# Performance work log

Measured on AMD Instinct MI355X. Metric: run time of the kernel, lower is better.

Reference implementation:

```python
import jax, jax.numpy as jnp
import numpy as np

B, BINS, EMBED, HID, IND = 1, 500, 1024, 512, 128
POOL, MC_CROP, HIC_CROP = 5, 50, 10


def setup_inputs() -> dict:
    key = jax.random.key(0)
    ks = jax.random.split(key, 10)
    def w(k, shape, fan_in):
        return (jax.random.normal(k, shape, jnp.float32) / np.sqrt(fan_in)).astype(jnp.float32)
    return dict(
        x=jax.random.normal(ks[0], (B, BINS, EMBED), jnp.float32),
        # project MLP
        p_w1=w(ks[1], (EMBED, HID), EMBED), p_b1=jnp.zeros((HID,), jnp.float32),
        p_w2=w(ks[2], (HID, HID), HID), p_b2=jnp.zeros((HID,), jnp.float32),
        # pairattn_cop stub: per-pair linears (micro at full res, hic after 5x5 avg-pool)
        micro_w=w(ks[3], (HID, IND), HID), micro_b=jnp.zeros((IND,), jnp.float32),
        hic_w=w(ks[4], (HID, IND), HID), hic_b=jnp.zeros((IND,), jnp.float32),
        # prediction heads
        head_mc_w=w(ks[5], (IND, 2), IND), head_mc_b=jnp.zeros((2,), jnp.float32),
        head_ih_w1=w(ks[6], (IND, IND // 2), IND), head_ih_b1=jnp.zeros((IND // 2,), jnp.float32),
        head_ih_w2=w(ks[7], (IND // 2, 2), IND // 2), head_ih_b2=jnp.zeros((2,), jnp.float32),
        head_hic_w=w(ks[8], (IND, 3), IND), head_hic_b=jnp.zeros((3,), jnp.float32),
    )


def reference(x, p_w1, p_b1, p_w2, p_b2, micro_w, micro_b, hic_w, hic_b,
              head_mc_w, head_mc_b, head_ih_w1, head_ih_b1, head_ih_w2, head_ih_b2,
              head_hic_w, head_hic_b):
    # project: Linear -> ReLU -> Linear
    h = jax.nn.relu(x @ p_w1 + p_b1) @ p_w2 + p_b2            # [B, bins, HID]
    # output_head: fused pairwise outer-sum mean + scaled elementwise dot
    xi = h[:, :, None, :]                                      # [B, bins, 1, HID]
    xj = h[:, None, :, :]                                      # [B, 1, bins, HID]
    pair = (xi + xj) * 0.5 + xi * xj * (1.0 / np.sqrt(HID))    # [B, bins, bins, HID]
    # pairattn_cop stub
    micro = pair @ micro_w + micro_b                           # [B, bins, bins, IND]
    nb = BINS // POOL
    hic_in = pair.reshape(B, nb, POOL, nb, POOL, HID).mean(axis=(2, 4))  # [B, nb, nb, HID]
    hic = hic_in @ hic_w + hic_b                               # [B, nb, nb, IND]
    # prediction heads with crops
    mc = micro[:, MC_CROP:-MC_CROP, MC_CROP:-MC_CROP, :]       # [B, 400, 400, IND]
    out_mc = mc @ head_mc_w + head_mc_b
    out_ih = jax.nn.relu(mc @ head_ih_w1 + head_ih_b1) @ head_ih_w2 + head_ih_b2
    hc = hic[:, HIC_CROP:-HIC_CROP, HIC_CROP:-HIC_CROP, :]     # [B, 80, 80, IND]
    out_hic = hc @ head_hic_w + head_hic_b
    return (out_mc, out_ih, micro, out_hic)
```

## Files before the change

kernel.cpp:

```cpp
#include <hip/hip_runtime.h>

#define BINS 500
#define HID  512
#define INDD 128
#define PAIR_S 0.044194173824159216f

#define OFF_MC    0
#define OFF_IH    320000
#define OFF_MICRO 640000
#define OFF_HIC   32640000

#define WS_U     0
#define WS_MWT   64000
#define WS_HBF   96768
#define WS_H     256000
#define WS_HBAR  512000
#define WS_HWT   563200
#define WS_W1CT  595968

typedef __bf16 bf16;
typedef bf16 bf16x4 __attribute__((ext_vector_type(4)));
typedef bf16 bf16x8 __attribute__((ext_vector_type(8)));
typedef float f32x4 __attribute__((ext_vector_type(4)));

__device__ __forceinline__ bf16x8 join8(bf16x4 lo, bf16x4 hi) {
  return __builtin_shufflevector(lo, hi, 0, 1, 2, 3, 4, 5, 6, 7);
}
__device__ __forceinline__ bf16x4 cvt4(float a, float b, float c, float d) {
  bf16x4 r; r[0] = (bf16)a; r[1] = (bf16)b; r[2] = (bf16)c; r[3] = (bf16)d; return r;
}

__global__ void zero_init(float* __restrict__ ws) {
  int idx = (blockIdx.x * 256 + threadIdx.x) * 4;
  float4 z = {0.f, 0.f, 0.f, 0.f};
  *(float4*)(ws + idx) = z;
  *(float4*)(ws + WS_H + idx) = z;
}

__global__ __launch_bounds__(256, 2)
void gemm_ks(const float* __restrict__ A, const float* __restrict__ B,
             const float* __restrict__ abias, float* __restrict__ C,
             int M, int N, int K_per, int a_relu, float scale) {
  __shared__ float a_lds[64][36];
  __shared__ float bt_lds[64][36];
  const int t = threadIdx.x;
  const int w = t >> 6, l = t & 63;
  const int lr = l & 15, g = l >> 4;
  const int r0 = blockIdx.x * 64, n0 = blockIdx.y * 64;
  const int kbase = blockIdx.z * K_per;
  f32x4 acc[4] = {};
  for (int kq = 0; kq < K_per; kq += 32) {
    const int k0 = kbase + kq;
    {
      int row = t >> 2, kc = (t & 3) * 8;
      int gr = r0 + row; gr = gr < M ? gr : M - 1;
      const float* src = A + (size_t)gr * K_per * gridDim.z + k0 + kc;
      float4 v0 = *(const float4*)src;
      float4 v1 = *(const float4*)(src + 4);
      if (abias) {
        const float* bp = abias + k0 + kc;
        v0.x += bp[0]; v0.y += bp[1]; v0.z += bp[2]; v0.w += bp[3];
        v1.x += bp[4]; v1.y += bp[5]; v1.z += bp[6]; v1.w += bp[7];
        if (a_relu) {
          v0.x = fmaxf(v0.x, 0.f); v0.y = fmaxf(v0.y, 0.f);
          v0.z = fmaxf(v0.z, 0.f); v0.w = fmaxf(v0.w, 0.f);
          v1.x = fmaxf(v1.x, 0.f); v1.y = fmaxf(v1.y, 0.f);
          v1.z = fmaxf(v1.z, 0.f); v1.w = fmaxf(v1.w, 0.f);
        }
      }
      *(float4*)&a_lds[row][kc]     = v0;
      *(float4*)&a_lds[row][kc + 4] = v1;
    }
    {
      int n = t & 63, ks = (t >> 6) * 8;
      const float* src = B + (size_t)(k0 + ks) * N + n0 + n;
      #pragma unroll
      for (int s = 0; s < 8; s++) bt_lds[n][ks + s] = src[(size_t)s * N];
    }
    __syncthreads();
    bf16x8 ahi, alo;
    {
      int row = w * 16 + lr;
      float4 u0 = *(const float4*)&a_lds[row][g * 8];
      float4 u1 = *(const float4*)&a_lds[row][g * 8 + 4];
      float v[8] = {u0.x, u0.y, u0.z, u0.w, u1.x, u1.y, u1.z, u1.w};
      #pragma unroll
      for (int e = 0; e < 8; e++) {
        bf16 h = (bf16)v[e];
        ahi[e] = h; alo[e] = (bf16)(v[e] - (float)h);
      }
    }
    #pragma unroll
    for (int fn = 0; fn < 4; fn++) {
      int col = fn * 16 + lr;
      float4 u0 = *(const float4*)&bt_lds[col][g * 8];
      float4 u1 = *(const float4*)&bt_lds[col][g * 8 + 4];
      float v[8] = {u0.x, u0.y, u0.z, u0.w, u1.x, u1.y, u1.z, u1.w};
      bf16x8 bhi, blo;
      #pragma unroll
      for (int e = 0; e < 8; e++) {
        bf16 h = (bf16)v[e];
        bhi[e] = h; blo[e] = (bf16)(v[e] - (float)h);
      }
      acc[fn] = __builtin_amdgcn_mfma_f32_16x16x32_bf16(ahi, bhi, acc[fn], 0, 0, 0);
      acc[fn] = __builtin_amdgcn_mfma_f32_16x16x32_bf16(ahi, blo, acc[fn], 0, 0, 0);
      acc[fn] = __builtin_amdgcn_mfma_f32_16x16x32_bf16(alo, bhi, acc[fn], 0, 0, 0);
    }
    __syncthreads();
  }
  #pragma unroll
  for (int fn = 0; fn < 4; fn++) {
    int col = n0 + fn * 16 + lr;
    #pragma unroll
    for (int r = 0; r < 4; r++) {
      int row = r0 + w * 16 + g * 4 + r;
      if (row < M) atomicAdd(&C[(size_t)row * N + col], acc[fn][r] * scale);
    }
  }
}

__global__ void post_h(const float* __restrict__ h, const float* __restrict__ b2,
                       const float* __restrict__ micro_w,
                       const float* __restrict__ hic_w, const float* __restrict__ w_ih1,
                       const float* __restrict__ w_mc, float* __restrict__ ws) {
  int g = blockIdx.x * 256 + threadIdx.x;
  if (g < 32000) {
    int e = g * 8, k = e & (HID - 1);
    float4 a0 = *(const float4*)(h + e),  a1 = *(const float4*)(h + e + 4);
    float4 c0 = *(const float4*)(b2 + k), c1 = *(const float4*)(b2 + k + 4);
    bf16x8 o;
    o[0] = (bf16)(a0.x + c0.x); o[1] = (bf16)(a0.y + c0.y);
    o[2] = (bf16)(a0.z + c0.z); o[3] = (bf16)(a0.w + c0.w);
    o[4] = (bf16)(a1.x + c1.x); o[5] = (bf16)(a1.y + c1.y);
    o[6] = (bf16)(a1.z + c1.z); o[7] = (bf16)(a1.w + c1.w);
    *(bf16x8*)((bf16*)(ws + WS_HBF) + e) = o;
  } else if (g < 40192) {
    int gg = (g - 32000) * 8;
    int n = gg >> 9, k = gg & 511;
    bf16x8 o;
    #pragma unroll
    for (int e = 0; e < 8; e++) o[e] = (bf16)(PAIR_S * micro_w[(size_t)(k + e) * INDD + n]);
    *(bf16x8*)((bf16*)(ws + WS_MWT) + gg) = o;
  } else if (g < 46592) {
    int gg = (g - 40192) * 8;
    int a = gg >> 9, k = gg & (HID - 1);
    const float* p = h + (size_t)(a * 5) * HID + k;
    float s[8] = {};
    #pragma unroll
    for (int r = 0; r < 5; r++) {
      float4 v0 = *(const float4*)(p + r * HID);
      float4 v1 = *(const float4*)(p + r * HID + 4);
      s[0] += v0.x; s[1] += v0.y; s[2] += v0.z; s[3] += v0.w;
      s[4] += v1.x; s[5] += v1.y; s[6] += v1.z; s[7] += v1.w;
    }
    float4 c0 = *(const float4*)(b2 + k), c1 = *(const float4*)(b2 + k + 4);
    float4 o0 = {s[0] * 0.2f + c0.x, s[1] * 0.2f + c0.y, s[2] * 0.2f + c0.z, s[3] * 0.2f + c0.w};
    float4 o1 = {s[4] * 0.2f + c1.x, s[5] * 0.2f + c1.y, s[6] * 0.2f + c1.z, s[7] * 0.2f + c1.w};
    *(float4*)(ws + WS_HBAR + gg)     = o0;
    *(float4*)(ws + WS_HBAR + gg + 4) = o1;
  } else if (g < 54784) {
    int gg = (g - 46592) * 8;
    int n = gg >> 9, k = gg & 511;
    bf16x8 o;
    #pragma unroll
    for (int e = 0; e < 8; e++) o[e] = (bf16)hic_w[(size_t)(k + e) * INDD + n];
    *(bf16x8*)((bf16*)(ws + WS_HWT) + gg) = o;
  } else if (g < 56064) {
    int gg = (g - 54784) * 8;
    int n = gg >> 7, k = gg & 127;
    bf16x8 o;
    #pragma unroll
    for (int e = 0; e < 8; e++) {
      float v = 0.f;
      if (n < 64) v = w_ih1[(k + e) * 64 + n];
      else if (n < 66) v = w_mc[(k + e) * 2 + (n - 64)];
      o[e] = (bf16)v;
    }
    *(bf16x8*)((bf16*)(ws + WS_W1CT) + gg) = o;
  } else if (g < 64064) {
    int gg = (g - 56064) * 8;
    float4 z = {0.f, 0.f, 0.f, 0.f};
    *(float4*)(ws + WS_U + gg)     = z;
    *(float4*)(ws + WS_U + gg + 4) = z;
  }
}

__global__ __launch_bounds__(256, 4)
void fused_micro(const float* __restrict__ wsf, const float* __restrict__ micro_b,
                 float* __restrict__ out) {
  __shared__ bf16 Ht[2][128 * 32];
  __shared__ bf16 Bt[2][128 * 32];
  const int t = threadIdx.x;
  const int wv = t >> 6, l = t & 63;
  const int wj = wv >> 1, wn = wv & 1;
  const int lr = l & 15, g = l >> 4;
  const int i  = blockIdx.x;
  const int j0 = blockIdx.y * 128;
  const bf16* Hbf = (const bf16*)(wsf + WS_HBF);
  const bf16* mwt = (const bf16*)(wsf + WS_MWT);
  const float* U  = wsf + WS_U;
  const int bn = t >> 1, bh = t & 1;
  const int arow   = l >> 2;
  const int achunk = (l & 3) ^ ((l >> 3) & 3);
  const bf16* hbi = Hbf + (size_t)i * HID;
  f32x4 acc[4][4] = {};

  #pragma unroll
  for (int q = 0; q < 2; q++) {
    int row = wv * 32 + q * 16 + arow;
    int jj = j0 + row; jj = jj < BINS ? jj : BINS - 1;
    __builtin_amdgcn_global_load_lds(
        (const __attribute__((address_space(1))) void*)(Hbf + (size_t)jj * HID + achunk * 8),
        (__attribute__((address_space(3))) void*)(&Ht[0][(wv * 32 + q * 16) * 32]),
        16, 0, 0);
  }
  {
    bf16x8 w0 = *(const bf16x8*)(mwt + (size_t)bn * HID + bh * 16);
    bf16x8 w1 = *(const bf16x8*)(mwt + (size_t)bn * HID + bh * 16 + 8);
    bf16x8 h0 = *(const bf16x8*)(hbi + bh * 16);
    bf16x8 h1 = *(const bf16x8*)(hbi + bh * 16 + 8);
    bf16x8 o0, o1;
    #pragma unroll
    for (int e = 0; e < 8; e++) o0[e] = (bf16)((float)h0[e] * (float)w0[e]);
    #pragma unroll
    for (int e = 0; e < 8; e++) o1[e] = (bf16)((float)h1[e] * (float)w1[e]);
    const int sw = (bn >> 1) & 3;
    *(bf16x8*)(&Bt[0][0] + bn * 32 + ((bh * 2)     ^ sw) * 8) = o0;
    *(bf16x8*)(&Bt[0][0] + bn * 32 + ((bh * 2 + 1) ^ sw) * 8) = o1;
  }
  asm volatile("s_waitcnt vmcnt(0) lgkmcnt(0)" ::: "memory");
  __builtin_amdgcn_s_barrier();

  int cur = 0;
  for (int kt = 0; kt < 16; kt++) {
    const bf16* htc = &Ht[cur][0];
    const bf16* btc = &Bt[cur][0];
    bf16x8 w0, w1, h0, h1;
    if (kt < 15) {
      const int kn = (kt + 1) * 32;
      w0 = *(const bf16x8*)(mwt + (size_t)bn * HID + kn + bh * 16);
      w1 = *(const bf16x8*)(mwt + (size_t)bn * HID + kn + bh * 16 + 8);
      h0 = *(const bf16x8*)(hbi + kn + bh * 16);
      h1 = *(const bf16x8*)(hbi + kn + bh * 16 + 8);
      #pragma unroll
      for (int q = 0; q < 2; q++) {
        int row = wv * 32 + q * 16 + arow;
        int jj = j0 + row; jj = jj < BINS ? jj : BINS - 1;
        __builtin_amdgcn_global_load_lds(
            (const __attribute__((address_space(1))) void*)(Hbf + (size_t)jj * HID + kn + achunk * 8),
            (__attribute__((address_space(3))) void*)(&Ht[cur ^ 1][(wv * 32 + q * 16) * 32]),
            16, 0, 0);
      }
      asm volatile("s_waitcnt vmcnt(6)" ::: "memory");
    } else {
      asm volatile("s_waitcnt vmcnt(0)" ::: "memory");
    }
    bf16x8 af[4], bfr[4];
    const int s = g ^ ((lr >> 1) & 3);
    #pragma unroll
    for (int fm = 0; fm < 4; fm++)
      af[fm] = *(const bf16x8*)(htc + (wj * 64 + fm * 16 + lr) * 32 + s * 8);
    #pragma unroll
    for (int fn = 0; fn < 4; fn++)
      bfr[fn] = *(const bf16x8*)(btc + (wn * 64 + fn * 16 + lr) * 32 + s * 8);
    #pragma unroll
    for (int fm = 0; fm < 4; fm++)
      #pragma unroll
      for (int fn = 0; fn < 4; fn++)
        acc[fm][fn] = __builtin_amdgcn_mfma_f32_16x16x32_bf16(af[fm], bfr[fn], acc[fm][fn], 0, 0, 0);
    if (kt < 15) {
      bf16x8 o0, o1;
      #pragma unroll
      for (int e = 0; e < 8; e++) o0[e] = (bf16)((float)h0[e] * (float)w0[e]);
      #pragma unroll
      for (int e = 0; e < 8; e++) o1[e] = (bf16)((float)h1[e] * (float)w1[e]);
      bf16* btn = &Bt[cur ^ 1][0];
      const int sw = (bn >> 1) & 3;
      *(bf16x8*)(btn + bn * 32 + ((bh * 2)     ^ sw) * 8) = o0;
      *(bf16x8*)(btn + bn * 32 + ((bh * 2 + 1) ^ sw) * 8) = o1;
    }
    asm volatile("s_waitcnt lgkmcnt(0)" ::: "memory");
    __builtin_amdgcn_s_barrier();
    cur ^= 1;
  }

  float Ui[4];
  #pragma unroll
  for (int fn = 0; fn < 4; fn++) {
    int n = wn * 64 + fn * 16 + lr;
    Ui[fn] = U[(size_t)i * INDD + n] + micro_b[n];
  }
  #pragma unroll
  for (int fm = 0; fm < 4; fm++) {
    #pragma unroll
    for (int r = 0; r < 4; r++) {
      int j = j0 + wj * 64 + fm * 16 + g * 4 + r;
      if (j < BINS) {
        const float* Uj = U + (size_t)j * INDD;
        size_t base = (size_t)OFF_MICRO + ((size_t)i * BINS + j) * INDD;
        #pragma unroll
        for (int fn = 0; fn < 4; fn++) {
          int n = wn * 64 + fn * 16 + lr;
          out[base + n] = acc[fm][fn][r] + Ui[fn] + Uj[n];
        }
      }
    }
  }
}

__global__ __launch_bounds__(256, 3)
void heads_direct(const float* __restrict__ micro, const float* __restrict__ wsf,
                  const float* __restrict__ b1, const float* __restrict__ w2,
                  const float* __restrict__ bmc, const float* __restrict__ b2,
                  float* __restrict__ out) {
  const int t = threadIdx.x;
  const int wv = t >> 6, l = t & 63;
  const int lr = l & 15, g = l >> 4;
  const int mm0 = blockIdx.x * 256;
  const bf16* w1c = (const bf16*)(wsf + WS_W1CT);
  int mrow[4];
  #pragma unroll
  for (int fm = 0; fm < 4; fm++) {
    int mm = mm0 + wv * 64 + fm * 16 + lr;
    mrow[fm] = 25050 + mm + 100 * (mm / 400);
  }
  f32x4 acc[4][5] = {};
  #pragma unroll
  for (int kt = 0; kt < 4; kt++) {
    const int k0 = kt * 32;
    bf16x8 bfr[5];
    #pragma unroll
    for (int fn = 0; fn < 5; fn++) {
      int q = fn * 16 + lr;
      bfr[fn] = *(const bf16x8*)(w1c + q * 128 + k0 + g * 8);
    }
    #pragma unroll
    for (int fm = 0; fm < 4; fm++) {
      const float* src = micro + (size_t)mrow[fm] * INDD + k0 + g * 8;
      float4 v0 = *(const float4*)src;
      float4 v1 = *(const float4*)(src + 4);
      bf16x8 af = join8(cvt4(v0.x, v0.y, v0.z, v0.w), cvt4(v1.x, v1.y, v1.z, v1.w));
      #pragma unroll
      for (int fn = 0; fn < 5; fn++)
        acc[fm][fn] = __builtin_amdgcn_mfma_f32_16x16x32_bf16(af, bfr[fn], acc[fm][fn], 0, 0, 0);
    }
  }
  float w2a[4], w2b[4], b1v[4];
  #pragma unroll
  for (int fn = 0; fn < 4; fn++) {
    int q = fn * 16 + lr;
    w2a[fn] = w2[q * 2]; w2b[fn] = w2[q * 2 + 1]; b1v[fn] = b1[q];
  }
  float bm = (lr < 2) ? bmc[lr] : 0.f;
  float b2a = b2[0], b2bv = b2[1];
  #pragma unroll
  for (int fm = 0; fm < 4; fm++) {
    #pragma unroll
    for (int r = 0; r < 4; r++) {
      int m = wv * 64 + fm * 16 + g * 4 + r;
      float s0 = 0.f, s1 = 0.f;
      #pragma unroll
      for (int fn = 0; fn < 4; fn++) {
        float v = fmaxf(acc[fm][fn][r] + b1v[fn], 0.f);
        s0 += v * w2a[fn]; s1 += v * w2b[fn];
      }
      #pragma unroll
      for (int mk = 1; mk < 16; mk <<= 1) {
        s0 += __shfl_xor(s0, mk);
        s1 += __shfl_xor(s1, mk);
      }
      size_t mo = (size_t)(mm0 + m);
      if (lr == 0) {
        out[OFF_IH + mo * 2]     = s0 + b2a;
        out[OFF_IH + mo * 2 + 1] = s1 + b2bv;
      }
      if (lr < 2) out[OFF_MC + mo * 2 + lr] = acc[fm][4][r] + bm;
    }
  }
}

__device__ __forceinline__ bf16x4 pair4(float4 a, float4 b) {
  bf16x4 r;
  r[0] = (bf16)((a.x + b.x) * 0.5f + a.x * b.x * PAIR_S);
  r[1] = (bf16)((a.y + b.y) * 0.5f + a.y * b.y * PAIR_S);
  r[2] = (bf16)((a.z + b.z) * 0.5f + a.z * b.z * PAIR_S);
  r[3] = (bf16)((a.w + b.w) * 0.5f + a.w * b.w * PAIR_S);
  return r;
}

__global__ __launch_bounds__(256, 2)
void hic_kernel(const float* __restrict__ hbar, const float* __restrict__ wsf,
                const float* __restrict__ hicb, const float* __restrict__ whic,
                const float* __restrict__ bhic, float* __restrict__ out) {
  __shared__ float ha_lds[16][36];
  __shared__ float hb_lds[16][36];
  __shared__ bf16 pair_lds[256][36];
  __shared__ bf16 bt_lds[128][36];
  const int t = threadIdx.x;
  const int wv = t >> 6, l = t & 63;
  const int lr = l & 15, g = l >> 4;
  const int a0 = 10 + blockIdx.x * 16, b0 = 10 + blockIdx.y * 16;
  const bf16* hwt = (const bf16*)(wsf + WS_HWT);
  f32x4 acc[4][8] = {};
  for (int kt = 0; kt < 16; kt++) {
    const int k0 = kt * 32;
    if (t < 64) {
      int row = t >> 2, c = (t & 3) * 8;
      const float* src = hbar + (size_t)(a0 + row) * HID + k0 + c;
      *(float4*)&ha_lds[row][c]     = *(const float4*)src;
      *(float4*)&ha_lds[row][c + 4] = *(const float4*)(src + 4);
    } else if (t < 128) {
      int tt = t - 64;
      int row = tt >> 2, c = (tt & 3) * 8;
      const float* src = hbar + (size_t)(b0 + row) * HID + k0 + c;
      *(float4*)&hb_lds[row][c]     = *(const float4*)src;
      *(float4*)&hb_lds[row][c + 4] = *(const float4*)(src + 4);
    } else {
      int tt = t - 128;
      #pragma unroll
      for (int rep = 0; rep < 4; rep++) {
        int chunk = tt * 4 + rep;
        int n = chunk >> 2, part = chunk & 3;
        bf16x8 v = *(const bf16x8*)(hwt + (size_t)n * HID + k0 + part * 8);
        *(bf16x4*)&bt_lds[n][part * 8]     = __builtin_shufflevector(v, v, 0, 1, 2, 3);
        *(bf16x4*)&bt_lds[n][part * 8 + 4] = __builtin_shufflevector(v, v, 4, 5, 6, 7);
      }
    }
    __syncthreads();
    {
      int m = t;
      const float* pa = &ha_lds[m >> 4][0];
      const float* pb = &hb_lds[m & 15][0];
      #pragma unroll
      for (int c = 0; c < 4; c++) {
        float4 av0 = *(const float4*)(pa + c * 8);
        float4 av1 = *(const float4*)(pa + c * 8 + 4);
        float4 bv0 = *(const float4*)(pb + c * 8);
        float4 bv1 = *(const float4*)(pb + c * 8 + 4);
        *(bf16x4*)&pair_lds[m][c * 8]     = pair4(av0, bv0);
        *(bf16x4*)&pair_lds[m][c * 8 + 4] = pair4(av1, bv1);
      }
    }
    __syncthreads();
    bf16x8 af[4], bfr[8];
    #pragma unroll
    for (int fm = 0; fm < 4; fm++) {
      int row = wv * 64 + fm * 16 + lr;
      af[fm] = join8(*(const bf16x4*)&pair_lds[row][g * 8],
                     *(const bf16x4*)&pair_lds[row][g * 8 + 4]);
    }
    #pragma unroll
    for (int fn = 0; fn < 8; fn++) {
      int col = fn * 16 + lr;
      bfr[fn] = join8(*(const bf16x4*)&bt_lds[col][g * 8],
                      *(const bf16x4*)&bt_lds[col][g * 8 + 4]);
    }
    #pragma unroll
    for (int fm = 0; fm < 4; fm++)
      #pragma unroll
      for (int fn = 0; fn < 8; fn++)
        acc[fm][fn] = __builtin_amdgcn_mfma_f32_16x16x32_bf16(af[fm], bfr[fn], acc[fm][fn], 0, 0, 0);
    __syncthreads();
  }
  float wh0[8], wh1[8], wh2[8], hbv[8];
  #pragma unroll
  for (int fn = 0; fn < 8; fn++) {
    int n = fn * 16 + lr;
    wh0[fn] = whic[n * 3]; wh1[fn] = whic[n * 3 + 1]; wh2[fn] = whic[n * 3 + 2];
    hbv[fn] = hicb[n];
  }
  float bh0 = bhic[0], bh1 = bhic[1], bh2 = bhic[2];
  #pragma unroll
  for (int fm = 0; fm < 4; fm++) {
    #pragma unroll
    for (int r = 0; r < 4; r++) {
      int m = wv * 64 + fm * 16 + g * 4 + r;
      float s0 = 0.f, s1 = 0.f, s2 = 0.f;
      #pragma unroll
      for (int fn = 0; fn < 8; fn++) {
        float v = acc[fm][fn][r] + hbv[fn];
        s0 += v * wh0[fn]; s1 += v * wh1[fn]; s2 += v * wh2[fn];
      }
      #pragma unroll
      for (int mk = 1; mk < 16; mk <<= 1) {
        s0 += __shfl_xor(s0, mk);
        s1 += __shfl_xor(s1, mk);
        s2 += __shfl_xor(s2, mk);
      }
      if (lr == 0) {
        int aa = a0 + (m >> 4) - 10, bb = b0 + (m & 15) - 10;
        size_t o = (size_t)OFF_HIC + (size_t)(aa * 80 + bb) * 3;
        out[o] = s0 + bh0; out[o + 1] = s1 + bh1; out[o + 2] = s2 + bh2;
      }
    }
  }
}

extern "C" void kernel_launch(void* const* d_in, const int* in_sizes, int n_in,
                              void* d_out, int out_size, void* d_ws, size_t ws_size,
                              hipStream_t stream) {
  (void)in_sizes; (void)n_in; (void)out_size; (void)ws_size;
  const float* x    = (const float*)d_in[0];
  const float* pw1  = (const float*)d_in[1];
  const float* pb1  = (const float*)d_in[2];
  const float* pw2  = (const float*)d_in[3];
  const float* pb2  = (const float*)d_in[4];
  const float* mw   = (const float*)d_in[5];
  const float* mb   = (const float*)d_in[6];
  const float* hw   = (const float*)d_in[7];
  const float* hb   = (const float*)d_in[8];
  const float* wmc  = (const float*)d_in[9];
  const float* bmc  = (const float*)d_in[10];
  const float* wih1 = (const float*)d_in[11];
  const float* bih1 = (const float*)d_in[12];
  const float* wih2 = (const float*)d_in[13];
  const float* bih2 = (const float*)d_in[14];
  const float* whic = (const float*)d_in[15];
  const float* bhic = (const float*)d_in[16];
  float* out = (float*)d_out;
  float* ws  = (float*)d_ws;

  zero_init<<<250, 256, 0, stream>>>(ws);
  gemm_ks<<<dim3(8, 8, 8), 256, 0, stream>>>(x, pw1, nullptr, ws, 500, 512, 128, 0, 1.f);
  gemm_ks<<<dim3(8, 8, 4), 256, 0, stream>>>(ws, pw2, pb1, ws + WS_H, 500, 512, 128, 1, 1.f);
  post_h<<<251, 256, 0, stream>>>(ws + WS_H, pb2, mw, hw, wih1, wmc, ws);
  gemm_ks<<<dim3(8, 2, 8), 256, 0, stream>>>(ws + WS_H, mw, pb2, ws + WS_U, 500, 128, 64, 0, 0.5f);
  fused_micro<<<dim3(500, 4), 256, 0, stream>>>(ws, mb, out);
  heads_direct<<<625, 256, 0, stream>>>(out + OFF_MICRO, ws, bih1, wih2, bmc, bih2, out);
  hic_kernel<<<dim3(5, 5), 256, 0, stream>>>(ws + WS_HBAR, ws, hb, whic, bhic, out);
}
```

Before: 157.5 us.

## Replace double-buffered LDS pipeline with single buffer and two barriers per k-step

Removes the double-buffered Ht/Bt shared-memory staging in fused_micro and uses single buffers. Each k-step now issues the async H tile loads and writes the scaled B tile, then syncs, computes the MFMAs and syncs again. This halves LDS use (which may allow more blocks per CU) and simplifies the waitcnt logic. In exchange, the next tile's global loads no longer overlap the current tile's MFMAs, and each iteration pays an extra barrier.

Result: no change. 156.3 us (-0.8%).

```diff
diff --git a/kernel.cpp b/kernel.cpp
--- a/kernel.cpp
+++ b/kernel.cpp
@@ -188,8 +188,8 @@
 __global__ __launch_bounds__(256, 4)
 void fused_micro(const float* __restrict__ wsf, const float* __restrict__ micro_b,
                  float* __restrict__ out) {
-  __shared__ bf16 Ht[2][128 * 32];
-  __shared__ bf16 Bt[2][128 * 32];
+  __shared__ bf16 Ht[128 * 32];
+  __shared__ bf16 Bt[128 * 32];
   const int t = threadIdx.x;
   const int wv = t >> 6, l = t & 63;
   const int wj = wv >> 1, wn = wv & 1;
@@ -205,83 +205,54 @@
   const bf16* hbi = Hbf + (size_t)i * HID;
   f32x4 acc[4][4] = {};
 
-  #pragma unroll
-  for (int q = 0; q < 2; q++) {
-    int row = wv * 32 + q * 16 + arow;
-    int jj = j0 + row; jj = jj < BINS ? jj : BINS - 1;
-    __builtin_amdgcn_global_load_lds(
-        (const __attribute__((address_space(1))) void*)(Hbf + (size_t)jj * HID + achunk * 8),
-        (__attribute__((address_space(3))) void*)(&Ht[0][(wv * 32 + q * 16) * 32]),
-        16, 0, 0);
-  }
-  {
-    bf16x8 w0 = *(const bf16x8*)(mwt + (size_t)bn * HID + bh * 16);
-    bf16x8 w1 = *(const bf16x8*)(mwt + (size_t)bn * HID + bh * 16 + 8);
-    bf16x8 h0 = *(const bf16x8*)(hbi + bh * 16);
-    bf16x8 h1 = *(const bf16x8*)(hbi + bh * 16 + 8);
-    bf16x8 o0, o1;
-    #pragma unroll
-    for (int e = 0; e < 8; e++) o0[e] = (bf16)((float)h0[e] * (float)w0[e]);
-    #pragma unroll
-    for (int e = 0; e < 8; e++) o1[e] = (bf16)((float)h1[e] * (float)w1[e]);
-    const int sw = (bn >> 1) & 3;
-    *(bf16x8*)(&Bt[0][0] + bn * 32 + ((bh * 2)     ^ sw) * 8) = o0;
-    *(bf16x8*)(&Bt[0][0] + bn * 32 + ((bh * 2 + 1) ^ sw) * 8) = o1;
-  }
-  asm volatile("s_waitcnt vmcnt(0) lgkmcnt(0)" ::: "memory");
-  __builtin_amdgcn_s_barrier();
-
-  int cur = 0;
+  bf16x8 w0 = *(const bf16x8*)(mwt + (size_t)bn * HID + bh * 16);
+  bf16x8 w1 = *(const bf16x8*)(mwt + (size_t)bn * HID + bh * 16 + 8);
+  bf16x8 h0 = *(const bf16x8*)(hbi + bh * 16);
+  bf16x8 h1 = *(const bf16x8*)(hbi + bh * 16 + 8);
+
   for (int kt = 0; kt < 16; kt++) {
-    const bf16* htc = &Ht[cur][0];
-    const bf16* btc = &Bt[cur][0];
-    bf16x8 w0, w1, h0, h1;
+    const int k0 = kt * 32;
+    #pragma unroll
+    for (int q = 0; q < 2; q++) {
+      int row = wv * 32 + q * 16 + arow;
+      int jj = j0 + row; jj = jj < BINS ? jj : BINS - 1;
+      __builtin_amdgcn_global_load_lds(
+          (const __attribute__((address_space(1))) void*)(Hbf + (size_t)jj * HID + k0 + achunk * 8),
+          (__attribute__((address_space(3))) void*)(Ht + (wv * 32 + q * 16) * 32),
+          16, 0, 0);
+    }
+    {
+      bf16x8 o0, o1;
+      #pragma unroll
+      for (int e = 0; e < 8; e++) o0[e] = (bf16)((float)h0[e] * (float)w0[e]);
+      #pragma unroll
+      for (int e = 0; e < 8; e++) o1[e] = (bf16)((float)h1[e] * (float)w1[e]);
+      const int sw = (bn >> 1) & 3;
+      *(bf16x8*)(Bt + bn * 32 + ((bh * 2)     ^ sw) * 8) = o0;
+      *(bf16x8*)(Bt + bn * 32 + ((bh * 2 + 1) ^ sw) * 8) = o1;
+    }
     if (kt < 15) {
-      const int kn = (kt + 1) * 32;
+      const int kn = k0 + 32;
       w0 = *(const bf16x8*)(mwt + (size_t)bn * HID + kn + bh * 16);
       w1 = *(const bf16x8*)(mwt + (size_t)bn * HID + kn + bh * 16 + 8);
       h0 = *(const bf16x8*)(hbi + kn + bh * 16);
       h1 = *(const bf16x8*)(hbi + kn + bh * 16 + 8);
-      #pragma unroll
-      for (int q = 0; q < 2; q++) {
-        int row = wv * 32 + q * 16 + arow;
-        int jj = j0 + row; jj = jj < BINS ? jj : BINS - 1;
-        __builtin_amdgcn_global_load_lds(
-            (const __attribute__((address_space(1))) void*)(Hbf + (size_t)jj * HID + kn + achunk * 8),
-            (__attribute__((address_space(3))) void*)(&Ht[cur ^ 1][(wv * 32 + q * 16) * 32]),
-            16, 0, 0);
-      }
-      asm volatile("s_waitcnt vmcnt(6)" ::: "memory");
-    } else {
-      asm volatile("s_waitcnt vmcnt(0)" ::: "memory");
-    }
+    }
+    __syncthreads();
     bf16x8 af[4], bfr[4];
     const int s = g ^ ((lr >> 1) & 3);
     #pragma unroll
     for (int fm = 0; fm < 4; fm++)
-      af[fm] = *(const bf16x8*)(htc + (wj * 64 + fm * 16 + lr) * 32 + s * 8);
+      af[fm] = *(const bf16x8*)(Ht + (wj * 64 + fm * 16 + lr) * 32 + s * 8);
     #pragma unroll
     for (int fn = 0; fn < 4; fn++)
-      bfr[fn] = *(const bf16x8*)(btc + (wn * 64 + fn * 16 + lr) * 32 + s * 8);
+      bfr[fn] = *(const bf16x8*)(Bt + (wn * 64 + fn * 16 + lr) * 32 + s * 8);
     #pragma unroll
     for (int fm = 0; fm < 4; fm++)
       #pragma unroll
       for (int fn = 0; fn < 4; fn++)
         acc[fm][fn] = __builtin_amdgcn_mfma_f32_16x16x32_bf16(af[fm], bfr[fn], acc[fm][fn], 0, 0, 0);
-    if (kt < 15) {
-      bf16x8 o0, o1;
-      #pragma unroll
-      for (int e = 0; e < 8; e++) o0[e] = (bf16)((float)h0[e] * (float)w0[e]);
-      #pragma unroll
-      for (int e = 0; e < 8; e++) o1[e] = (bf16)((float)h1[e] * (float)w1[e]);
-      bf16* btn = &Bt[cur ^ 1][0];
-      const int sw = (bn >> 1) & 3;
-      *(bf16x8*)(btn + bn * 32 + ((bh * 2)     ^ sw) * 8) = o0;
-      *(bf16x8*)(btn + bn * 32 + ((bh * 2 + 1) ^ sw) * 8) = o1;
-    }
-    asm volatile("s_waitcnt lgkmcnt(0)" ::: "memory");
-    __builtin_amdgcn_s_barrier();
-    cur ^= 1;
+    __syncthreads();
   }
 
   float Ui[4];
```

## Prefetch B-operand inputs two stages ahead and prioritize MFMA issue in fused_micro

Applied to the files above, without the earlier changes.

Restructures the K-loop software pipeline in fused_micro. The weight and h values used to build the scaled B tile are now loaded into registers two K-steps ahead. The next B tile is written to LDS before the MFMA block, and the MFMA block is wrapped in s_setprio to raise wave priority. The hand-tuned s_waitcnt/s_barrier pairs become __syncthreads, and launch bounds drop from 4 to 3 waves per SIMD to leave room for the extra prefetch registers. The aim is to hide global load latency behind matrix work. The risks are lower occupancy, and a fence in __syncthreads that may wait on all outstanding loads, including the prefetches.

New measurement: 158.1 us. About the same (+0.4%).

```diff
diff --git a/kernel.cpp b/kernel.cpp
--- a/kernel.cpp
+++ b/kernel.cpp
@@ -185,7 +185,7 @@
   }
 }
 
-__global__ __launch_bounds__(256, 4)
+__global__ __launch_bounds__(256, 3)
 void fused_micro(const float* __restrict__ wsf, const float* __restrict__ micro_b,
                  float* __restrict__ out) {
   __shared__ bf16 Ht[2][128 * 32];
@@ -203,8 +203,24 @@
   const int arow   = l >> 2;
   const int achunk = (l & 3) ^ ((l >> 3) & 3);
   const bf16* hbi = Hbf + (size_t)i * HID;
+  const bf16* wsrc = mwt + (size_t)bn * HID + bh * 16;
+  const bf16* hsrc = hbi + bh * 16;
   f32x4 acc[4][4] = {};
 
+  {
+    bf16x8 w0 = *(const bf16x8*)(wsrc);
+    bf16x8 w1 = *(const bf16x8*)(wsrc + 8);
+    bf16x8 h0 = *(const bf16x8*)(hsrc);
+    bf16x8 h1 = *(const bf16x8*)(hsrc + 8);
+    bf16x8 o0, o1;
+    #pragma unroll
+    for (int e = 0; e < 8; e++) o0[e] = (bf16)((float)h0[e] * (float)w0[e]);
+    #pragma unroll
+    for (int e = 0; e < 8; e++) o1[e] = (bf16)((float)h1[e] * (float)w1[e]);
+    const int sw = (bn >> 1) & 3;
+    *(bf16x8*)(&Bt[0][0] + bn * 32 + ((bh * 2)     ^ sw) * 8) = o0;
+    *(bf16x8*)(&Bt[0][0] + bn * 32 + ((bh * 2 + 1) ^ sw) * 8) = o1;
+  }
   #pragma unroll
   for (int q = 0; q < 2; q++) {
     int row = wv * 32 + q * 16 + arow;
@@ -214,34 +230,24 @@
         (__attribute__((address_space(3))) void*)(&Ht[0][(wv * 32 + q * 16) * 32]),
         16, 0, 0);
   }
-  {
-    bf16x8 w0 = *(const bf16x8*)(mwt + (size_t)bn * HID + bh * 16);
-    bf16x8 w1 = *(const bf16x8*)(mwt + (size_t)bn * HID + bh * 16 + 8);
-    bf16x8 h0 = *(const bf16x8*)(hbi + bh * 16);
-    bf16x8 h1 = *(const bf16x8*)(hbi + bh * 16 + 8);
-    bf16x8 o0, o1;
-    #pragma unroll
-    for (int e = 0; e < 8; e++) o0[e] = (bf16)((float)h0[e] * (float)w0[e]);
-    #pragma unroll
-    for (int e = 0; e < 8; e++) o1[e] = (bf16)((float)h1[e] * (float)w1[e]);
-    const int sw = (bn >> 1) & 3;
-    *(bf16x8*)(&Bt[0][0] + bn * 32 + ((bh * 2)     ^ sw) * 8) = o0;
-    *(bf16x8*)(&Bt[0][0] + bn * 32 + ((bh * 2 + 1) ^ sw) * 8) = o1;
-  }
-  asm volatile("s_waitcnt vmcnt(0) lgkmcnt(0)" ::: "memory");
-  __builtin_amdgcn_s_barrier();
+  bf16x8 wu0 = *(const bf16x8*)(wsrc + 32);
+  bf16x8 wu1 = *(const bf16x8*)(wsrc + 40);
+  bf16x8 hu0 = *(const bf16x8*)(hsrc + 32);
+  bf16x8 hu1 = *(const bf16x8*)(hsrc + 40);
+  __syncthreads();
 
   int cur = 0;
   for (int kt = 0; kt < 16; kt++) {
-    const bf16* htc = &Ht[cur][0];
-    const bf16* btc = &Bt[cur][0];
-    bf16x8 w0, w1, h0, h1;
+    bf16x8 wp0, wp1, hp0, hp1;
+    if (kt < 14) {
+      const int kf = (kt + 2) * 32;
+      wp0 = *(const bf16x8*)(wsrc + kf);
+      wp1 = *(const bf16x8*)(wsrc + kf + 8);
+      hp0 = *(const bf16x8*)(hsrc + kf);
+      hp1 = *(const bf16x8*)(hsrc + kf + 8);
+    }
     if (kt < 15) {
       const int kn = (kt + 1) * 32;
-      w0 = *(const bf16x8*)(mwt + (size_t)bn * HID + kn + bh * 16);
-      w1 = *(const bf16x8*)(mwt + (size_t)bn * HID + kn + bh * 16 + 8);
-      h0 = *(const bf16x8*)(hbi + kn + bh * 16);
-      h1 = *(const bf16x8*)(hbi + kn + bh * 16 + 8);
       #pragma unroll
       for (int q = 0; q < 2; q++) {
         int row = wv * 32 + q * 16 + arow;
@@ -251,36 +257,35 @@
             (__attribute__((address_space(3))) void*)(&Ht[cur ^ 1][(wv * 32 + q * 16) * 32]),
             16, 0, 0);
       }
-      asm volatile("s_waitcnt vmcnt(6)" ::: "memory");
-    } else {
-      asm volatile("s_waitcnt vmcnt(0)" ::: "memory");
     }
     bf16x8 af[4], bfr[4];
     const int s = g ^ ((lr >> 1) & 3);
     #pragma unroll
     for (int fm = 0; fm < 4; fm++)
-      af[fm] = *(const bf16x8*)(htc + (wj * 64 + fm * 16 + lr) * 32 + s * 8);
+      af[fm] = *(const bf16x8*)(&Ht[cur][0] + (wj * 64 + fm * 16 + lr) * 32 + s * 8);
     #pragma unroll
     for (int fn = 0; fn < 4; fn++)
-      bfr[fn] = *(const bf16x8*)(btc + (wn * 64 + fn * 16 + lr) * 32 + s * 8);
-    #pragma unroll
-    for (int fm = 0; fm < 4; fm++)
-      #pragma unroll
-      for (int fn = 0; fn < 4; fn++)
-        acc[fm][fn] = __builtin_amdgcn_mfma_f32_16x16x32_bf16(af[fm], bfr[fn], acc[fm][fn], 0, 0, 0);
+      bfr[fn] = *(const bf16x8*)(&Bt[cur][0] + (wn * 64 + fn * 16 + lr) * 32 + s * 8);
     if (kt < 15) {
       bf16x8 o0, o1;
       #pragma unroll
-      for (int e = 0; e < 8; e++) o0[e] = (bf16)((float)h0[e] * (float)w0[e]);
-      #pragma unroll
-      for (int e = 0; e < 8; e++) o1[e] = (bf16)((float)h1[e] * (float)w1[e]);
+      for (int e = 0; e < 8; e++) o0[e] = (bf16)((float)hu0[e] * (float)wu0[e]);
+      #pragma unroll
+      for (int e = 0; e < 8; e++) o1[e] = (bf16)((float)hu1[e] * (float)wu1[e]);
       bf16* btn = &Bt[cur ^ 1][0];
       const int sw = (bn >> 1) & 3;
       *(bf16x8*)(btn + bn * 32 + ((bh * 2)     ^ sw) * 8) = o0;
       *(bf16x8*)(btn + bn * 32 + ((bh * 2 + 1) ^ sw) * 8) = o1;
     }
-    asm volatile("s_waitcnt lgkmcnt(0)" ::: "memory");
-    __builtin_amdgcn_s_barrier();
+    __builtin_amdgcn_s_setprio(1);
+    #pragma unroll
+    for (int fm = 0; fm < 4; fm++)
+      #pragma unroll
+      for (int fn = 0; fn < 4; fn++)
+        acc[fm][fn] = __builtin_amdgcn_mfma_f32_16x16x32_bf16(af[fm], bfr[fn], acc[fm][fn], 0, 0, 0);
+    __builtin_amdgcn_s_setprio(0);
+    __syncthreads();
+    wu0 = wp0; wu1 = wp1; hu0 = hp0; hu1 = hp1;
     cur ^= 1;
   }
 
```
